# Kernel tuning notes

Hardware: AMD Instinct MI355X
Metric: run time of the kernel (lower is better)

## Reference

```python
import jax, jax.numpy as jnp
import numpy as np

B, T, C, H = 2, 2048, 2048, 16
HD = C // H  # 128 head dim
ROPE_BASE = 10000.0


def setup_inputs() -> dict:
    key = jax.random.key(0)
    k0, k1, k2 = jax.random.split(key, 3)
    x = jax.random.normal(k0, (B, T, C), dtype=jnp.float32)
    W_attn = jax.random.normal(k1, (C, 3 * C), dtype=jnp.float32) * 0.02
    b_attn = jnp.zeros((3 * C,), dtype=jnp.float32)
    W_proj = jax.random.normal(k2, (C, C), dtype=jnp.float32) * 0.02
    b_proj = jnp.zeros((C,), dtype=jnp.float32)
    # freqs_cis = exp(i * t * theta_j), represented as (cos, sin), shape [T, HD//2]
    inv_freq = 1.0 / (ROPE_BASE ** (jnp.arange(0, HD, 2, dtype=jnp.float32) / HD))
    freqs = jnp.outer(jnp.arange(T, dtype=jnp.float32), inv_freq)
    return {"x": x, "W_attn": W_attn, "b_attn": b_attn, "W_proj": W_proj,
            "b_proj": b_proj, "cos": jnp.cos(freqs), "sin": jnp.sin(freqs)}


def _apply_rope(v, cos, sin):
    # v: [B, T, H, HD]; pairs (v[..., 2i], v[..., 2i+1]) rotated by angle freqs[t, i]
    vr = v.reshape(v.shape[:-1] + (-1, 2))
    x0, x1 = vr[..., 0], vr[..., 1]
    c = cos[None, :, None, :]  # [1, T, 1, HD//2]
    s = sin[None, :, None, :]
    o0 = x0 * c - x1 * s
    o1 = x0 * s + x1 * c
    return jnp.stack([o0, o1], axis=-1).reshape(v.shape)


def reference(x, W_attn, b_attn, W_proj, b_proj, cos, sin):
    Bv, Tv, Cv = x.shape
    qkv = x @ W_attn + b_attn                      # [B, T, 3C]
    q, k, v = jnp.split(qkv, 3, axis=-1)
    q = q.reshape(Bv, Tv, H, HD)
    k = k.reshape(Bv, Tv, H, HD)
    v = v.reshape(Bv, Tv, H, HD)
    q = _apply_rope(q, cos, sin)
    k = _apply_rope(k, cos, sin)
    scale = 1.0 / jnp.sqrt(jnp.float32(HD))
    att = jnp.einsum('bqhd,bkhd->bhqk', q, k) * scale
    causal = jnp.tril(jnp.ones((Tv, Tv), dtype=bool))
    att = jnp.where(causal[None, None], att, jnp.finfo(att.dtype).min)
    att = jax.nn.softmax(att, axis=-1)
    y = jnp.einsum('bhqk,bkhd->bqhd', att, v).reshape(Bv, Tv, Cv)
    return y @ W_proj + b_proj
```

## Files before the change

kernel.cpp:

```cpp
#include <hip/hip_runtime.h>

typedef unsigned short u16;
typedef __attribute__((ext_vector_type(8))) short short8;
typedef __attribute__((ext_vector_type(4))) float f32x4;

#define TSEQ 2048
#define NHEAD 16
#define HDIM 128

__device__ __forceinline__ u16 f2bf(float x) {
    unsigned u = __float_as_uint(x);
    return (u16)((u + 0x7fffu + ((u >> 16) & 1u)) >> 16);
}
__device__ __forceinline__ float b2f(u16 h) {
    return __uint_as_float(((unsigned)h) << 16);
}
__device__ __forceinline__ void async16(const void* g, void* l) {
    __builtin_amdgcn_global_load_lds((__attribute__((address_space(1))) void*)(void*)g,
                                     (__attribute__((address_space(3))) void*)l, 16, 0, 0);
}
__device__ __forceinline__ f32x4 zero4() {
    f32x4 z = {0.f, 0.f, 0.f, 0.f};
    return z;
}

template <int CTRL>
__device__ __forceinline__ float dppf(float x) {
    return __int_as_float(__builtin_amdgcn_mov_dpp(__float_as_int(x), CTRL, 0xf, 0xf, true));
}
__device__ __forceinline__ float dpp_max16(float x) {
    x = fmaxf(x, dppf<0xB1>(x));
    x = fmaxf(x, dppf<0x4E>(x));
    x = fmaxf(x, dppf<0x141>(x));
    x = fmaxf(x, dppf<0x140>(x));
    return x;
}
__device__ __forceinline__ float dpp_sum16(float x) {
    x += dppf<0xB1>(x);
    x += dppf<0x4E>(x);
    x += dppf<0x141>(x);
    x += dppf<0x140>(x);
    return x;
}

__global__ void cast_bf16(const float4* __restrict__ in, ushort4* __restrict__ out, int n4) {
    int i = blockIdx.x * 256 + threadIdx.x;
    if (i < n4) {
        float4 v = in[i];
        ushort4 o;
        o.x = f2bf(v.x); o.y = f2bf(v.y); o.z = f2bf(v.z); o.w = f2bf(v.w);
        out[i] = o;
    }
}

__global__ void transpose_cast(const float* __restrict__ in, u16* __restrict__ out, int K, int N) {
    __shared__ float tile[64][65];
    int n0 = blockIdx.x * 64, k0 = blockIdx.y * 64;
    int tx = threadIdx.x & 63, ty = threadIdx.x >> 6;
#pragma unroll
    for (int i = 0; i < 16; i++) {
        int r = ty + i * 4;
        tile[r][tx] = in[(size_t)(k0 + r) * N + n0 + tx];
    }
    __syncthreads();
#pragma unroll
    for (int i = 0; i < 16; i++) {
        int r = ty + i * 4;
        out[(size_t)(n0 + r) * K + k0 + tx] = f2bf(tile[tx][r]);
    }
}

template <int MODE>
__global__ __launch_bounds__(256) void gemm_bt(
    const u16* __restrict__ A, const u16* __restrict__ Bt, const float* __restrict__ bias,
    float* __restrict__ outf, u16* __restrict__ qb, u16* __restrict__ kb, u16* __restrict__ vT,
    const float* __restrict__ cosp, const float* __restrict__ sinp,
    int M, int N, int K) {
    __shared__ __align__(16) u16 smem[8704];
    u16* As = smem;
    u16* Bs = smem + 4096;
    const int tid = threadIdx.x;
    const int wave = tid >> 6, lane = tid & 63;
    const int low = lane & 15, quad = lane >> 4;
    const int m0 = blockIdx.y * 128, n0 = blockIdx.x * 128;
    const int wm = (wave >> 1) * 64, wn = (wave & 1) * 64;
    const int ldr = lane >> 2;
    const int ldc = (lane & 3) * 8;

    f32x4 acc[4][4];
#pragma unroll
    for (int i = 0; i < 4; i++)
#pragma unroll
        for (int j = 0; j < 4; j++) acc[i][j] = zero4();

    for (int k0 = 0; k0 < K; k0 += 32) {
#pragma unroll
        for (int c = 0; c < 2; ++c) {
            const int chunk = wave * 2 + c;
            const int row = chunk * 16 + ldr;
            async16(A + (size_t)(m0 + row) * K + k0 + ldc, As + chunk * 512);
            async16(Bt + (size_t)(n0 + row) * K + k0 + ldc, Bs + chunk * 512);
        }
        __syncthreads();
        short8 af[4], bfv[4];
#pragma unroll
        for (int i = 0; i < 4; i++) af[i] = *(const short8*)(As + (wm + i * 16 + low) * 32 + quad * 8);
#pragma unroll
        for (int j = 0; j < 4; j++) bfv[j] = *(const short8*)(Bs + (wn + j * 16 + low) * 32 + quad * 8);
#pragma unroll
        for (int i = 0; i < 4; i++)
#pragma unroll
            for (int j = 0; j < 4; j++)
                acc[i][j] = __builtin_amdgcn_mfma_f32_16x16x32_bf16(af[i], bfv[j], acc[i][j], 0, 0, 0);
        __syncthreads();
    }

    if (MODE == 1) {
#pragma unroll
        for (int j = 0; j < 4; j++) {
            const int ng = n0 + wn + j * 16 + low;
            const float bv = bias[ng];
#pragma unroll
            for (int i = 0; i < 4; i++) {
                const int rbase = m0 + wm + i * 16 + quad * 4;
#pragma unroll
                for (int r = 0; r < 4; r++)
                    outf[(size_t)(rbase + r) * N + ng] = acc[i][j][r] + bv;
            }
        }
        return;
    }

    const int which = n0 >> 11;
    const int h = (n0 & 2047) >> 7;
    const int b = m0 >> 11, t0 = m0 & 2047;
    float bv[4];
#pragma unroll
    for (int j = 0; j < 4; j++) bv[j] = bias[n0 + wn + j * 16 + low];
    u16* epi = smem;

    if (which < 2) {
        u16* dst = (which == 0 ? qb : kb) + (((size_t)(b * NHEAD + h)) * TSEQ + t0) * HDIM;
#pragma unroll
        for (int pass = 0; pass < 2; pass++) {
            if ((wave >> 1) == pass) {
#pragma unroll
                for (int i = 0; i < 4; i++)
#pragma unroll
                    for (int j = 0; j < 4; j++)
#pragma unroll
                        for (int r = 0; r < 4; r++)
                            epi[(i * 16 + quad * 4 + r) * 136 + wn + j * 16 + low] =
                                f2bf(acc[i][j][r] + bv[j]);
            }
            __syncthreads();
            const int row = tid >> 2, dp = (tid & 3) * 32;
            const int t = t0 + pass * 64 + row;
            u16 vals[32];
#pragma unroll
            for (int q = 0; q < 4; q++)
                *(short8*)(vals + q * 8) = *(const short8*)(epi + row * 136 + dp + q * 8);
            float cs4[16], sn4[16];
#pragma unroll
            for (int q = 0; q < 4; q++) {
                *(float4*)(cs4 + q * 4) = *(const float4*)(cosp + (size_t)t * 64 + (dp >> 1) + q * 4);
                *(float4*)(sn4 + q * 4) = *(const float4*)(sinp + (size_t)t * 64 + (dp >> 1) + q * 4);
            }
            u16 outv[32];
#pragma unroll
            for (int p = 0; p < 16; p++) {
                float x0 = b2f(vals[2 * p]), x1 = b2f(vals[2 * p + 1]);
                outv[2 * p] = f2bf(x0 * cs4[p] - x1 * sn4[p]);
                outv[2 * p + 1] = f2bf(x0 * sn4[p] + x1 * cs4[p]);
            }
            u16* dr = dst + (size_t)(pass * 64 + row) * HDIM + dp;
#pragma unroll
            for (int q = 0; q < 4; q++)
                *(short8*)(dr + q * 8) = *(const short8*)(outv + q * 8);
            __syncthreads();
        }
    } else {
        u16* dst = vT + ((size_t)(b * NHEAD + h)) * HDIM * TSEQ + t0;
#pragma unroll
        for (int pass = 0; pass < 2; pass++) {
            if ((wave & 1) == pass) {
#pragma unroll
                for (int i = 0; i < 4; i++)
#pragma unroll
                    for (int j = 0; j < 4; j++)
#pragma unroll
                        for (int r = 0; r < 4; r++)
                            epi[(j * 16 + low) * 136 + wm + i * 16 + quad * 4 + r] =
                                f2bf(acc[i][j][r] + bv[j]);
            }
            __syncthreads();
            const int drow = tid >> 2, tc = (tid & 3) * 32;
            u16* dr = dst + (size_t)(pass * 64 + drow) * TSEQ + tc;
#pragma unroll
            for (int q = 0; q < 4; q++)
                *(short8*)(dr + q * 8) = *(const short8*)(epi + drow * 136 + tc + q * 8);
            __syncthreads();
        }
    }
}

__global__ __launch_bounds__(256) void flash_attn(const u16* __restrict__ qb, const u16* __restrict__ kb,
                                                  const u16* __restrict__ vT, u16* __restrict__ y) {
    __shared__ u16 Ks[64 * 128];
    __shared__ u16 Vs[128 * 64];
    __shared__ u16 Ps[4][16 * 72];
    const int tid = threadIdx.x;
    const int wave = tid >> 6, lane = tid & 63;
    const int low = lane & 15, quad = lane >> 4;
    const int bh = blockIdx.x;
    const int qt = 31 - blockIdx.y;
    const int q0 = qt * 64 + wave * 16;
    const float scale2 = 0.08838834764831845f * 1.44269504088896f;

    const u16* Qp = qb + ((size_t)bh * TSEQ + q0) * HDIM;
    short8 qf[4];
#pragma unroll
    for (int c = 0; c < 4; c++) qf[c] = *(const short8*)(Qp + (size_t)low * HDIM + c * 32 + quad * 8);

    f32x4 o[8];
#pragma unroll
    for (int d = 0; d < 8; d++) o[d] = zero4();
    float m_i[4], l_i[4];
#pragma unroll
    for (int r = 0; r < 4; r++) { m_i[r] = -1e30f; l_i[r] = 0.f; }

    const u16* Kb = kb + (size_t)bh * TSEQ * HDIM;
    const u16* Vb = vT + (size_t)bh * HDIM * TSEQ;
    u16* Pw = &Ps[wave][0];
    const int ntiles = qt + 1;

    const int krow = tid >> 4, kchunk = tid & 15;
    const int vrow = tid >> 3, vchunk = tid & 7;

    for (int kt = 0; kt < ntiles; ++kt) {
        const int kv0 = kt * 64;
#pragma unroll
        for (int j = 0; j < 4; j++) {
            const int row = j * 16 + krow;
            const int gc = kchunk ^ (row & 7);
            async16(Kb + (size_t)(kv0 + row) * HDIM + gc * 8, Ks + row * 128 + kchunk * 8);
        }
#pragma unroll
        for (int j = 0; j < 4; j++) {
            const int d = j * 32 + vrow;
            const int gc = vchunk ^ (d & 7);
            async16(Vb + (size_t)d * TSEQ + kv0 + gc * 8, Vs + d * 64 + vchunk * 8);
        }
        __syncthreads();

        f32x4 s[4];
#pragma unroll
        for (int h = 0; h < 4; h++) s[h] = zero4();
#pragma unroll
        for (int h = 0; h < 4; h++) {
            const int row = h * 16 + low;
#pragma unroll
            for (int c = 0; c < 4; c++) {
                const int cc = c * 4 + quad;
                short8 kf = *(const short8*)(Ks + row * 128 + (cc ^ (row & 7)) * 8);
                s[h] = __builtin_amdgcn_mfma_f32_16x16x32_bf16(qf[c], kf, s[h], 0, 0, 0);
            }
        }

        float alpha[4];
#pragma unroll
        for (int r = 0; r < 4; r++) {
            const int qg = q0 + quad * 4 + r;
            float sv[4];
#pragma unroll
            for (int h = 0; h < 4; h++)
                sv[h] = (kv0 + h * 16 + low <= qg) ? s[h][r] * scale2 : -1e30f;
            float mx = fmaxf(fmaxf(sv[0], sv[1]), fmaxf(sv[2], sv[3]));
            mx = dpp_max16(mx);
            float mnew = fmaxf(m_i[r], mx);
            alpha[r] = exp2f(m_i[r] - mnew);
            m_i[r] = mnew;
            float p0 = exp2f(sv[0] - mnew);
            float p1 = exp2f(sv[1] - mnew);
            float p2 = exp2f(sv[2] - mnew);
            float p3 = exp2f(sv[3] - mnew);
            float rs = (p0 + p1) + (p2 + p3);
            rs = dpp_sum16(rs);
            l_i[r] = l_i[r] * alpha[r] + rs;
            const int prow = (quad * 4 + r) * 72;
            Pw[prow + low] = f2bf(p0);
            Pw[prow + 16 + low] = f2bf(p1);
            Pw[prow + 32 + low] = f2bf(p2);
            Pw[prow + 48 + low] = f2bf(p3);
        }
        __threadfence_block();

#pragma unroll
        for (int d = 0; d < 8; ++d)
#pragma unroll
            for (int r = 0; r < 4; r++) o[d][r] *= alpha[r];

#pragma unroll
        for (int kc = 0; kc < 2; kc++) {
            short8 pf = *(const short8*)(Pw + low * 72 + kc * 32 + quad * 8);
#pragma unroll
            for (int dd = 0; dd < 8; ++dd) {
                const int vr = dd * 16 + low;
                const int cc = kc * 4 + quad;
                short8 vf = *(const short8*)(Vs + vr * 64 + (cc ^ (vr & 7)) * 8);
                o[dd] = __builtin_amdgcn_mfma_f32_16x16x32_bf16(pf, vf, o[dd], 0, 0, 0);
            }
        }
        __syncthreads();
    }

    const int b = bh >> 4, h = bh & 15;
#pragma unroll
    for (int r = 0; r < 4; r++) {
        float inv = 1.0f / l_i[r];
        size_t row = (size_t)(b * TSEQ + q0 + quad * 4 + r);
        u16* yp = y + row * 2048 + h * HDIM;
#pragma unroll
        for (int d = 0; d < 8; ++d) yp[d * 16 + low] = f2bf(o[d][r] * inv);
    }
}

extern "C" void kernel_launch(void* const* d_in, const int* in_sizes, int n_in,
                              void* d_out, int out_size, void* d_ws, size_t ws_size,
                              hipStream_t stream) {
    const float* x = (const float*)d_in[0];
    const float* Wa = (const float*)d_in[1];
    const float* ba = (const float*)d_in[2];
    const float* Wp = (const float*)d_in[3];
    const float* bp = (const float*)d_in[4];
    const float* cs = (const float*)d_in[5];
    const float* sn = (const float*)d_in[6];
    float* out = (float*)d_out;

    u16* xb = (u16*)d_ws;
    u16* Wab = xb + 8388608;
    u16* Wpb = Wab + 12582912;
    u16* qb = Wpb + 4194304;
    u16* kb = qb + 8388608;
    u16* vT = kb + 8388608;
    u16* y = xb;

    cast_bf16<<<8192, 256, 0, stream>>>((const float4*)x, (ushort4*)xb, 2097152);
    transpose_cast<<<dim3(96, 32), 256, 0, stream>>>(Wa, Wab, 2048, 6144);
    transpose_cast<<<dim3(32, 32), 256, 0, stream>>>(Wp, Wpb, 2048, 2048);
    gemm_bt<0><<<dim3(48, 32), 256, 0, stream>>>(xb, Wab, ba, nullptr, qb, kb, vT, cs, sn, 4096, 6144, 2048);
    flash_attn<<<dim3(32, 32), 256, 0, stream>>>(qb, kb, vT, y);
    gemm_bt<1><<<dim3(16, 32), 256, 0, stream>>>(y, Wpb, bp, out, nullptr, nullptr, nullptr, nullptr, nullptr, 4096, 2048, 2048);
}
```

Baseline: 446.3 us.

## Replace QKV GEMM with 256x256-tile 8-wave ping-pong pipelined kernel

```diff
diff --git a/kernel.cpp b/kernel.cpp
--- a/kernel.cpp
+++ b/kernel.cpp
@@ -199,6 +199,217 @@
 #pragma unroll
             for (int q = 0; q < 4; q++)
                 *(short8*)(dr + q * 8) = *(const short8*)(epi + drow * 136 + tc + q * 8);
+            __syncthreads();
+        }
+    }
+}
+
+
+#define PH_PRE()                                           \
+    {                                                      \
+        __builtin_amdgcn_s_barrier();                      \
+        asm volatile("s_waitcnt lgkmcnt(0)" ::: "memory"); \
+        __builtin_amdgcn_sched_barrier(0);                 \
+        __builtin_amdgcn_s_setprio(1);                     \
+    }
+#define PH_POST()                       \
+    {                                   \
+        __builtin_amdgcn_s_setprio(0);  \
+        __builtin_amdgcn_s_barrier();   \
+    }
+#define PH_POSTV(N)                                            \
+    {                                                          \
+        __builtin_amdgcn_s_setprio(0);                         \
+        asm volatile("s_waitcnt vmcnt(" #N ")" ::: "memory");  \
+        __builtin_amdgcn_s_barrier();                          \
+    }
+
+#define STAGE(GP, GROW0, LB, KT)                                                                     \
+    {                                                                                                \
+        const int ktc__ = ((KT) < NT ? (KT) : NT - 1);                                               \
+        const u16* g0__ = (GP) + (size_t)((GROW0) + wave * 16 + grow) * (size_t)K + ktc__ * 64 +     \
+                          gslot * 8;                                                                 \
+        u16* l0__ = (LB) + wave * 1024;                                                              \
+        async16(g0__, l0__);                                                                         \
+        async16(g0__ + (size_t)8 * K, l0__ + 512);                                                   \
+    }
+
+#define LDA4(BASE, MB)                                                              \
+    {                                                                               \
+        _Pragma("unroll") for (int mm = 0; mm < 4; ++mm) {                          \
+            a[mm][0] = *(const short8*)((BASE) + aoff0 + ((MB) + mm) * 1024);       \
+            a[mm][1] = *(const short8*)((BASE) + aoff1 + ((MB) + mm) * 1024);       \
+        }                                                                           \
+    }
+#define LDB2(BASE, NB)                                                              \
+    {                                                                               \
+        _Pragma("unroll") for (int nn = 0; nn < 2; ++nn) {                          \
+            b[(NB) + nn][0] = *(const short8*)((BASE) + boff0 + ((NB) + nn) * 1024);\
+            b[(NB) + nn][1] = *(const short8*)((BASE) + boff1 + ((NB) + nn) * 1024);\
+        }                                                                           \
+    }
+#define MFQ(MB, NB)                                                                                   \
+    {                                                                                                 \
+        _Pragma("unroll") for (int mm = 0; mm < 4; ++mm) _Pragma("unroll") for (int nn = 0; nn < 2;   \
+                                                                                ++nn) {               \
+            acc[(MB) + mm][(NB) + nn] = __builtin_amdgcn_mfma_f32_16x16x32_bf16(                      \
+                a[mm][0], b[(NB) + nn][0], acc[(MB) + mm][(NB) + nn], 0, 0, 0);                       \
+            acc[(MB) + mm][(NB) + nn] = __builtin_amdgcn_mfma_f32_16x16x32_bf16(                      \
+                a[mm][1], b[(NB) + nn][1], acc[(MB) + mm][(NB) + nn], 0, 0, 0);                       \
+        }                                                                                             \
+    }
+
+__global__ __launch_bounds__(512, 2) void gemm256(
+    const u16* __restrict__ A, const u16* __restrict__ Bt, const float* __restrict__ bias,
+    u16* __restrict__ qb, u16* __restrict__ kb, u16* __restrict__ vT,
+    const float* __restrict__ cosp, const float* __restrict__ sinp,
+    int M, int N, int K) {
+    extern __shared__ u16 sm[];
+    u16* const smA0 = sm;
+    u16* const smB0 = sm + 16384;
+    u16* const smA1 = sm + 32768;
+    u16* const smB1 = sm + 49152;
+
+    const int tid = threadIdx.x;
+    const int wave = tid >> 6, lane = tid & 63;
+    const int low = lane & 15, quad = lane >> 4;
+    const int wr = wave >> 2, wc = wave & 3;
+    const int m0 = blockIdx.y * 256, n0 = blockIdx.x * 256;
+    const int NT = K >> 6;
+
+    const int grow = lane >> 3;
+    const int gslot = (lane & 7) ^ grow;
+
+    const int swz = low & 7;
+    const int arow = (wr * 128 + low) * 64;
+    const int brow = (wc * 64 + low) * 64;
+    const int aoff0 = arow + ((0 + quad) ^ swz) * 8;
+    const int aoff1 = arow + ((4 + quad) ^ swz) * 8;
+    const int boff0 = brow + ((0 + quad) ^ swz) * 8;
+    const int boff1 = brow + ((4 + quad) ^ swz) * 8;
+
+    f32x4 acc[8][4];
+#pragma unroll
+    for (int i = 0; i < 8; i++)
+#pragma unroll
+        for (int j = 0; j < 4; j++) acc[i][j] = zero4();
+    short8 a[4][2], b[4][2];
+
+    STAGE(A, m0, smA0, 0);
+    STAGE(A, m0 + 128, smA0 + 8192, 0);
+    STAGE(Bt, n0, smB0, 0);
+    STAGE(Bt, n0 + 128, smB0 + 8192, 0);
+    STAGE(A, m0, smA1, 1);
+    STAGE(A, m0 + 128, smA1 + 8192, 1);
+    asm volatile("s_waitcnt vmcnt(4)" ::: "memory");
+    __builtin_amdgcn_s_barrier();
+
+#pragma unroll 1
+    for (int it = 0; it < (NT >> 1); ++it) {
+        const int e = it * 2;
+        LDA4(smA0, 0);
+        LDB2(smB0, 0);
+        STAGE(Bt, n0, smB1, e + 1);
+        PH_PRE(); MFQ(0, 0); PH_POST();
+        LDB2(smB0, 2);
+        STAGE(Bt, n0 + 128, smB1 + 8192, e + 1);
+        PH_PRE(); MFQ(0, 2); PH_POST();
+        LDA4(smA0, 4);
+        PH_PRE(); MFQ(4, 2); PH_POST();
+        STAGE(A, m0, smA0, e + 2);
+        PH_PRE(); MFQ(4, 0); PH_POSTV(2);
+        LDA4(smA1, 0);
+        LDB2(smB1, 0);
+        STAGE(A, m0 + 128, smA0 + 8192, e + 2);
+        PH_PRE(); MFQ(0, 0); PH_POST();
+        LDB2(smB1, 2);
+        STAGE(Bt, n0, smB0, e + 2);
+        PH_PRE(); MFQ(0, 2); PH_POST();
+        LDA4(smA1, 4);
+        STAGE(Bt, n0 + 128, smB0 + 8192, e + 2);
+        PH_PRE(); MFQ(4, 2); PH_POST();
+        STAGE(A, m0, smA1, e + 3);
+        STAGE(A, m0 + 128, smA1 + 8192, e + 3);
+        PH_PRE(); MFQ(4, 0); PH_POSTV(4);
+    }
+
+    asm volatile("s_waitcnt vmcnt(0)" ::: "memory");
+    __syncthreads();
+
+    const int which = n0 >> 11;
+    const int h0 = (n0 & 2047) >> 7;
+    const int bb = m0 >> 11, t0 = m0 & 2047;
+    float bvv[4];
+#pragma unroll
+    for (int nn = 0; nn < 4; ++nn) bvv[nn] = bias[n0 + wc * 64 + nn * 16 + low];
+
+    if (which < 2) {
+        u16* dstb = (which == 0 ? qb : kb);
+        u16* epi = sm;
+#pragma unroll
+        for (int hh = 0; hh < 2; ++hh) {
+            if ((wc >> 1) == hh) {
+#pragma unroll
+                for (int mm = 0; mm < 8; ++mm)
+#pragma unroll
+                    for (int nn = 0; nn < 4; ++nn)
+#pragma unroll
+                        for (int rr = 0; rr < 4; ++rr)
+                            epi[(wr * 128 + mm * 16 + quad * 4 + rr) * 136 +
+                                (wc & 1) * 64 + nn * 16 + low] = f2bf(acc[mm][nn][rr] + bvv[nn]);
+            }
+            __syncthreads();
+            {
+                const int row = tid >> 1, dh = (tid & 1) * 64;
+                const int t = t0 + row;
+                u16* dr = dstb + (((size_t)(bb * NHEAD + h0 + hh)) * TSEQ + t) * HDIM + dh;
+                u16 vals[64];
+#pragma unroll
+                for (int qq = 0; qq < 8; ++qq)
+                    *(short8*)(vals + qq * 8) = *(const short8*)(epi + row * 136 + dh + qq * 8);
+                float csv[32], snv[32];
+#pragma unroll
+                for (int qq = 0; qq < 8; ++qq) {
+                    *(float4*)(csv + qq * 4) =
+                        *(const float4*)(cosp + (size_t)t * 64 + (dh >> 1) + qq * 4);
+                    *(float4*)(snv + qq * 4) =
+                        *(const float4*)(sinp + (size_t)t * 64 + (dh >> 1) + qq * 4);
+                }
+                u16 ov[64];
+#pragma unroll
+                for (int pp = 0; pp < 32; ++pp) {
+                    float x0 = b2f(vals[2 * pp]), x1 = b2f(vals[2 * pp + 1]);
+                    ov[2 * pp] = f2bf(x0 * csv[pp] - x1 * snv[pp]);
+                    ov[2 * pp + 1] = f2bf(x0 * snv[pp] + x1 * csv[pp]);
+                }
+#pragma unroll
+                for (int qq = 0; qq < 8; ++qq)
+                    *(short8*)(dr + qq * 8) = *(const short8*)(ov + qq * 8);
+            }
+            __syncthreads();
+        }
+    } else {
+        u16* epi = sm;
+#pragma unroll
+        for (int hh = 0; hh < 2; ++hh) {
+            if ((wc >> 1) == hh) {
+#pragma unroll
+                for (int mm = 0; mm < 8; ++mm)
+#pragma unroll
+                    for (int nn = 0; nn < 4; ++nn)
+#pragma unroll
+                        for (int rr = 0; rr < 4; ++rr)
+                            epi[((wc & 1) * 64 + nn * 16 + low) * 264 +
+                                wr * 128 + mm * 16 + quad * 4 + rr] = f2bf(acc[mm][nn][rr] + bvv[nn]);
+            }
+            __syncthreads();
+            {
+                const int dd = tid >> 2, tc = (tid & 3) * 64;
+                u16* dr = vT + ((size_t)(bb * NHEAD + h0 + hh) * HDIM + dd) * TSEQ + t0 + tc;
+#pragma unroll
+                for (int qq = 0; qq < 8; ++qq)
+                    *(short8*)(dr + qq * 8) = *(const short8*)(epi + dd * 264 + tc + qq * 8);
+            }
             __syncthreads();
         }
     }
@@ -345,10 +556,17 @@
     u16* vT = kb + 8388608;
     u16* y = xb;
 
+    static bool attr_set = false;
+    if (!attr_set) {
+        hipFuncSetAttribute(reinterpret_cast<const void*>(gemm256),
+                            hipFuncAttributeMaxDynamicSharedMemorySize, 131072);
+        attr_set = true;
+    }
+
     cast_bf16<<<8192, 256, 0, stream>>>((const float4*)x, (ushort4*)xb, 2097152);
     transpose_cast<<<dim3(96, 32), 256, 0, stream>>>(Wa, Wab, 2048, 6144);
     transpose_cast<<<dim3(32, 32), 256, 0, stream>>>(Wp, Wpb, 2048, 2048);
-    gemm_bt<0><<<dim3(48, 32), 256, 0, stream>>>(xb, Wab, ba, nullptr, qb, kb, vT, cs, sn, 4096, 6144, 2048);
+    gemm256<<<dim3(24, 16), 512, 131072, stream>>>(xb, Wab, ba, qb, kb, vT, cs, sn, 4096, 6144, 2048);
     flash_attn<<<dim3(32, 32), 256, 0, stream>>>(qb, kb, vT, y);
     gemm_bt<1><<<dim3(16, 32), 256, 0, stream>>>(y, Wpb, bp, out, nullptr, nullptr, nullptr, nullptr, nullptr, 4096, 2048, 2048);
 }
```

After: 423.4 us. -5.1%, faster.
